# Kernel tuning notes

Measured on AMD Instinct MI355X. Metric: run time of the kernel, lower is better.

## Reference

```python
import jax, jax.numpy as jnp
import numpy as np


def mha(x, mask, wq, bq, wk, bk, wv, bv, wo, bo, n_heads):
    # Flaubert/XLM MultiHeadAttention (eval mode, dropout = identity).
    bs, qlen, dim = x.shape
    dph = dim // n_heads

    def split_heads(t):  # (bs, qlen, dim) -> (bs, n_heads, qlen, dph)
        return t.reshape(bs, qlen, n_heads, dph).transpose(0, 2, 1, 3)

    q = split_heads(x @ wq + bq) / jnp.sqrt(jnp.asarray(dph, x.dtype))
    k = split_heads(x @ wk + bk)
    v = split_heads(x @ wv + bv)

    scores = jnp.einsum('bhqd,bhkd->bhqk', q, k)  # (bs, h, qlen, klen)
    neg = jnp.finfo(scores.dtype).min
    scores = jnp.where((mask == 0)[:, None, None, :], neg, scores)
    weights = jax.nn.softmax(scores, axis=-1)
    ctx = jnp.einsum('bhqk,bhkd->bhqd', weights, v)
    ctx = ctx.transpose(0, 2, 1, 3).reshape(bs, qlen, dim)
    return ctx @ wo + bo


def setup_inputs() -> dict:
    key = jax.random.key(0)
    ks = jax.random.split(key, 20)
    bs, slen = 4, 1024
    d0, d1 = 192, 66
    std = 0.02
    inp = {
        'x': jax.random.normal(ks[0], (bs, slen, d0), jnp.float32),
        'y': jax.random.normal(ks[1], (bs, slen, d1), jnp.float32),
        'mask0': jax.random.randint(ks[2], (bs, slen), 0, 2, jnp.int32),
        'mask1': jax.random.randint(ks[3], (bs, slen), 0, 2, jnp.int32),
    }
    names0 = ['q0', 'k0', 'v0', 'o0']
    names1 = ['q1', 'k1', 'v1', 'o1']
    for i, n in enumerate(names0):
        inp[n + '_w'] = jax.random.normal(ks[4 + i], (d0, d0), jnp.float32) * std
        inp[n + '_b'] = jnp.zeros((d0,), jnp.float32)
    for i, n in enumerate(names1):
        inp[n + '_w'] = jax.random.normal(ks[8 + i], (d1, d1), jnp.float32) * std
        inp[n + '_b'] = jnp.zeros((d1,), jnp.float32)
    return inp


def reference(x, y, mask0, mask1,
              q0_w, q0_b, k0_w, k0_b, v0_w, v0_b, o0_w, o0_b,
              q1_w, q1_b, k1_w, k1_b, v1_w, v1_b, o1_w, o1_b):
    out0 = mha(x, mask0, q0_w, q0_b, k0_w, k0_b, v0_w, v0_b, o0_w, o0_b, n_heads=16)
    out1 = mha(y, mask1, q1_w, q1_b, k1_w, k1_b, v1_w, v1_b, o1_w, o1_b, n_heads=11)
    return (out0, out1)
```

## Files before the change

kernel.cpp:

```cpp
#include <hip/hip_runtime.h>
#include <math.h>


#define BS 4
#define SLEN 1024

#define Q0_OFF 0
#define C0_OFF 786432
#define Q1_OFF 1572864
#define C1_OFF 1843200
#define K0H_OFF 2113536
#define V0T_OFF 2506752
#define K1H_OFF 2899968
#define V1T_OFF 3080192
#define CMAP0_OFF 3215360
#define CMAP1_OFF 3219456
#define CNT_OFF 3223552

#define OUT0_SIZE 786432

#if __has_builtin(__builtin_amdgcn_exp2f)
#define EXP2(x) __builtin_amdgcn_exp2f(x)
#else
#define EXP2(x) __expf((x) * 0.69314718056f)
#endif

typedef _Float16 f16x2 __attribute__((ext_vector_type(2)));
typedef _Float16 f16x4 __attribute__((ext_vector_type(4)));
typedef _Float16 f16x8 __attribute__((ext_vector_type(8)));
typedef float f32x4 __attribute__((ext_vector_type(4)));

union F16x8U { f16x8 v8; f16x4 v4[2]; };

__global__ __launch_bounds__(256) void compact_kernel(
    const int* __restrict__ mask0, const int* __restrict__ mask1,
    int* __restrict__ cmap0, int* __restrict__ cmap1, int* __restrict__ cnts)
{
  __shared__ int sS[256];
  __shared__ int sTot;
  const int inst = blockIdx.x >> 2, b = blockIdx.x & 3;
  const int* m = (inst ? mask1 : mask0) + b * SLEN;
  int* cmap = (inst ? cmap1 : cmap0) + b * SLEN;
  const int tid = threadIdx.x;

  int mv[4], s4 = 0;
#pragma unroll
  for (int i = 0; i < 4; ++i) { mv[i] = m[tid * 4 + i] ? 1 : 0; s4 += mv[i]; }
  sS[tid] = s4;
  __syncthreads();
  for (int off = 1; off < 256; off <<= 1) {
    const int v = sS[tid];
    const int add = (tid >= off) ? sS[tid - off] : 0;
    __syncthreads();
    sS[tid] = v + add;
    __syncthreads();
  }
  if (tid == 255) sTot = sS[255];
  __syncthreads();
  const int tot = sTot;
  int u = tid ? sS[tid - 1] : 0;
#pragma unroll
  for (int i = 0; i < 4; ++i) {
    const int s = tid * 4 + i;
    cmap[s] = mv[i] ? u : tot + (s - u);
    u += mv[i];
  }
  if (tid == 0) cnts[blockIdx.x] = tot;
}

__device__ __forceinline__ void mfma_chunk(const _Float16* sA, const _Float16* sWT,
                                           int wv, int lane, f32x4 acc[4])
{
  const int col = lane & 15, grp = lane >> 4;
#pragma unroll
  for (int ks = 0; ks < 2; ++ks) {
    const f16x8 bf = *(const f16x8*)(sWT + (wv * 16 + col) * 72 + ks * 32 + grp * 8);
#pragma unroll
    for (int mt = 0; mt < 4; ++mt) {
      const f16x8 af = *(const f16x8*)(sA + (mt * 16 + col) * 72 + ks * 32 + grp * 8);
      acc[mt] = __builtin_amdgcn_mfma_f32_16x16x32_f16(af, bf, acc[mt], 0, 0, 0);
    }
  }
}

__device__ __forceinline__ void mfma_chunk_split(
    const _Float16* sAh, const _Float16* sAl,
    const _Float16* sWTh, const _Float16* sWTl,
    int wv, int lane, f32x4 acc[4])
{
  const int col = lane & 15, grp = lane >> 4;
#pragma unroll
  for (int ks = 0; ks < 2; ++ks) {
    const int boff = (wv * 16 + col) * 72 + ks * 32 + grp * 8;
    const f16x8 bh = *(const f16x8*)(sWTh + boff);
    const f16x8 bl = *(const f16x8*)(sWTl + boff);
#pragma unroll
    for (int mt = 0; mt < 4; ++mt) {
      const int aoff = (mt * 16 + col) * 72 + ks * 32 + grp * 8;
      const f16x8 ah = *(const f16x8*)(sAh + aoff);
      const f16x8 al = *(const f16x8*)(sAl + aoff);
      acc[mt] = __builtin_amdgcn_mfma_f32_16x16x32_f16(ah, bh, acc[mt], 0, 0, 0);
      acc[mt] = __builtin_amdgcn_mfma_f32_16x16x32_f16(ah, bl, acc[mt], 0, 0, 0);
      acc[mt] = __builtin_amdgcn_mfma_f32_16x16x32_f16(al, bh, acc[mt], 0, 0, 0);
    }
  }
}

template <int DIM>
__device__ __forceinline__ void stage_chunk(const float* __restrict__ A, int row0,
                                            int kc, const float* __restrict__ W,
                                            int col0, _Float16* sA, _Float16* sWT,
                                            int tid)
{
  for (int idx = tid; idx < 2048; idx += 256) {
    const int m = idx >> 5, k = (idx & 31) * 2;
    float2 v = make_float2(0.f, 0.f);
    if (kc + k < DIM) v = *(const float2*)(A + (size_t)(row0 + m) * DIM + kc + k);
    *(f16x2*)(sA + m * 72 + k) = (f16x2){(_Float16)v.x, (_Float16)v.y};
  }
  for (int idx = tid; idx < 2048; idx += 256) {
    const int k = idx >> 5, n = (idx & 31) * 2;
    float2 v = make_float2(0.f, 0.f);
    if (kc + k < DIM && col0 + n < DIM)
      v = *(const float2*)(W + (size_t)(kc + k) * DIM + col0 + n);
    sWT[n * 72 + k] = (_Float16)v.x;
    sWT[(n + 1) * 72 + k] = (_Float16)v.y;
  }
}

template <int DIM>
__device__ __forceinline__ void stage_chunk_split(
    const float* __restrict__ A, int row0, int kc,
    const float* __restrict__ W, int col0,
    _Float16* sAh, _Float16* sAl, _Float16* sWTh, _Float16* sWTl, int tid)
{
  for (int idx = tid; idx < 2048; idx += 256) {
    const int m = idx >> 5, k = (idx & 31) * 2;
    float2 v = make_float2(0.f, 0.f);
    if (kc + k < DIM) v = *(const float2*)(A + (size_t)(row0 + m) * DIM + kc + k);
    const _Float16 hx = (_Float16)v.x, hy = (_Float16)v.y;
    *(f16x2*)(sAh + m * 72 + k) = (f16x2){hx, hy};
    *(f16x2*)(sAl + m * 72 + k) =
        (f16x2){(_Float16)(v.x - (float)hx), (_Float16)(v.y - (float)hy)};
  }
  for (int idx = tid; idx < 2048; idx += 256) {
    const int k = idx >> 5, n = (idx & 31) * 2;
    float2 v = make_float2(0.f, 0.f);
    if (kc + k < DIM && col0 + n < DIM)
      v = *(const float2*)(W + (size_t)(kc + k) * DIM + col0 + n);
    const _Float16 hx = (_Float16)v.x, hy = (_Float16)v.y;
    sWTh[n * 72 + k] = hx;
    sWTh[(n + 1) * 72 + k] = hy;
    sWTl[n * 72 + k] = (_Float16)(v.x - (float)hx);
    sWTl[(n + 1) * 72 + k] = (_Float16)(v.y - (float)hy);
  }
}

template <int DIM, int H, int DPH, int NT, int NCH, int KST>
__device__ void qkv_impl(int bid, const float* __restrict__ X,
                         const float* __restrict__ qw, const float* __restrict__ qb,
                         const float* __restrict__ kw, const float* __restrict__ kb,
                         const float* __restrict__ vw, const float* __restrict__ vb,
                         float* __restrict__ qo, _Float16* __restrict__ kh,
                         _Float16* __restrict__ vth, const int* __restrict__ cmap,
                         char* smem)
{
  const int mt64 = bid & 63;
  const int rest = bid >> 6;
  const int mat = rest / NT;
  const int nt = rest % NT;
  const int row0 = mt64 * 64, col0 = nt * 64;

  const float* W = (mat == 0) ? qw : (mat == 1) ? kw : vw;
  const float* B = (mat == 0) ? qb : (mat == 1) ? kb : vb;
  const float scale = (mat == 0) ? (1.44269504089f / sqrtf((float)DPH)) : 1.0f;

  _Float16* sA = (_Float16*)smem;
  _Float16* sWT = sA + 64 * 72;

  const int tid = threadIdx.x;
  const int wv = tid >> 6, lane = tid & 63;
  f32x4 acc[4] = {{0.f,0.f,0.f,0.f},{0.f,0.f,0.f,0.f},{0.f,0.f,0.f,0.f},{0.f,0.f,0.f,0.f}};

  for (int c = 0; c < NCH; ++c) {
    __syncthreads();
    stage_chunk<DIM>(X, row0, c * 64, W, col0, sA, sWT, tid);
    __syncthreads();
    mfma_chunk(sA, sWT, wv, lane, acc);
  }

  const int col = lane & 15, grp = lane >> 4;
  const int cidx = col0 + wv * 16 + col;
  if (cidx < DIM) {
    const float bias = B[cidx];
    const int h = cidx / DPH, d = cidx % DPH;
#pragma unroll
    for (int mt = 0; mt < 4; ++mt) {
#pragma unroll
      for (int r = 0; r < 4; ++r) {
        const int m = row0 + mt * 16 + grp * 4 + r;
        const int b = m >> 10, s = m & 1023;
        const float v = acc[mt][r] + bias;
        const int bh = b * H + h;
        if (mat == 0) {
          qo[(size_t)((bh << 10) + s) * DPH + d] = v * scale;
        } else {
          const int sp = cmap[(b << 10) + s];
          if (mat == 1)
            kh[(size_t)((bh << 10) + sp) * KST + d] = (_Float16)v;
          else
            vth[((size_t)(bh * DPH + d) << 10) + sp] = (_Float16)v;
        }
      }
    }
  }
}

__global__ __launch_bounds__(256) void qkv_kernel(
    const float* __restrict__ x, const float* __restrict__ y,
    const float* __restrict__ q0w, const float* __restrict__ q0b,
    const float* __restrict__ k0w, const float* __restrict__ k0b,
    const float* __restrict__ v0w, const float* __restrict__ v0b,
    const float* __restrict__ q1w, const float* __restrict__ q1b,
    const float* __restrict__ k1w, const float* __restrict__ k1b,
    const float* __restrict__ v1w, const float* __restrict__ v1b,
    float* __restrict__ ws)
{
  extern __shared__ char smem[];
  _Float16* hws = (_Float16*)ws;
  const int* cmap0 = (const int*)(ws + CMAP0_OFF);
  const int* cmap1 = (const int*)(ws + CMAP1_OFF);
  const int bid = blockIdx.x;
  if (bid < 576)
    qkv_impl<192, 16, 12, 3, 3, 12>(bid, x, q0w, q0b, k0w, k0b, v0w, v0b,
                                    ws + Q0_OFF, hws + 2 * (size_t)K0H_OFF,
                                    hws + 2 * (size_t)V0T_OFF, cmap0, smem);
  else
    qkv_impl<66, 11, 6, 2, 2, 8>(bid - 576, y, q1w, q1b, k1w, k1b, v1w, v1b,
                                 ws + Q1_OFF, hws + 2 * (size_t)K1H_OFF,
                                 hws + 2 * (size_t)V1T_OFF, cmap1, smem);
}

template <int H, int DPH, int SKP>
__device__ void attn_impl(int bid, const float* __restrict__ qg,
                          const _Float16* __restrict__ kh,
                          const _Float16* __restrict__ vth,
                          const int* __restrict__ cnts,
                          float* __restrict__ ctx, char* smem)
{
  constexpr int CH = 128;
  constexpr int KBUF = CH * SKP + 32;
  constexpr int VST = 136;

  _Float16* sK = (_Float16*)smem;
  _Float16* sVT = sK + 2 * KBUF;

  const int bh = bid >> 4;
  const int b = bh / H;
  const int h = bh % H;
  const int tid = threadIdx.x;

  const float* qb_ = qg + (size_t)bh * SLEN * DPH;
  const _Float16* kb_ = kh + (size_t)bh * SLEN * SKP;
  const _Float16* vb_ = vth + ((size_t)bh * DPH << 10);
  const int cnt = cnts[b];
  const int nch = (cnt + CH - 1) >> 7;

  if (tid < 64) sK[(tid >> 5) * KBUF + CH * SKP + (tid & 31)] = (_Float16)0.f;

  const int wave = tid >> 6, lane = tid & 63;
  const int col = lane & 15, grp = lane >> 4;
  const int qtile = (bid & 15) * 4 + wave;

  f16x4 aq;
  {
    const int qrow = qtile * 16 + col;
#pragma unroll
    for (int j = 0; j < 4; ++j) {
      const int d = grp * 4 + j;
      aq[j] = (d < DPH) ? (_Float16)qb_[(size_t)qrow * DPH + d] : (_Float16)0.f;
    }
  }

  constexpr int kN = CH * SKP / 8;
  constexpr int vN = DPH * 16;
  const int vd = tid >> 4, vq = tid & 15;
  uint4 pk, pv;
  auto prefetch = [&](int cc) {
    if (tid < kN) pk = ((const uint4*)(kb_ + (size_t)cc * CH * SKP))[tid];
    if (tid < vN) pv = ((const uint4*)(vb_ + ((size_t)vd << 10) + cc * CH))[vq];
  };
  auto commit = [&](int pb) {
    if (tid < kN) ((uint4*)(sK + pb * KBUF))[tid] = pk;
    if (tid < vN) *(uint4*)(sVT + (pb * DPH + vd) * VST + vq * 8) = pv;
  };

  prefetch(0);
  commit(0);
  __syncthreads();

  f32x4 Oacc[2] = {{0.f,0.f,0.f,0.f},{0.f,0.f,0.f,0.f}};
  float lsum = 0.f;
  const int de = (col < DPH) ? col : 0;

#pragma unroll 1
  for (int c = 0; c < nch; ++c) {
    const int p = c & 1;
    if (c + 1 < nch) prefetch(c + 1);

    const _Float16* sKp = sK + p * KBUF;
    const _Float16* sVp = sVT + p * DPH * VST;
    const int keyr = c * CH + grp * 4;

#pragma unroll
    for (int kt = 0; kt < CH / 16; ++kt) {
      const f16x4 kf = *(const f16x4*)(sKp + (kt * 16 + col) * SKP + grp * 4);
      const int k0 = keyr + kt * 16;
      const f32x4 biasv = {(k0 < cnt) ? 0.f : -100.f,
                           (k0 + 1 < cnt) ? 0.f : -100.f,
                           (k0 + 2 < cnt) ? 0.f : -100.f,
                           (k0 + 3 < cnt) ? 0.f : -100.f};
      const f32x4 S = __builtin_amdgcn_mfma_f32_16x16x16f16(kf, aq, biasv,
                                                            0, 0, 0);
      const float e0 = EXP2(S[0]), e1 = EXP2(S[1]);
      const float e2 = EXP2(S[2]), e3 = EXP2(S[3]);
      lsum += (e0 + e1) + (e2 + e3);
      const f16x4 pf = {(_Float16)e0, (_Float16)e1, (_Float16)e2, (_Float16)e3};
      const f16x4 vf = *(const f16x4*)(sVp + de * VST + kt * 16 + grp * 4);
      Oacc[kt & 1] = __builtin_amdgcn_mfma_f32_16x16x16f16(pf, vf, Oacc[kt & 1],
                                                           0, 0, 0);
    }

    if (c + 1 < nch) commit(p ^ 1);
    __syncthreads();
  }

  f32x4 Osum;
#pragma unroll
  for (int r = 0; r < 4; ++r) Osum[r] = Oacc[0][r] + Oacc[1][r];
  float lred = lsum;
  lred += __shfl_xor(lred, 16);
  lred += __shfl_xor(lred, 32);
  float lq[4];
#pragma unroll
  for (int r = 0; r < 4; ++r) lq[r] = __shfl(lred, grp * 4 + r);
  if (col < DPH) {
    const int qrow0 = qtile * 16;
#pragma unroll
    for (int r = 0; r < 4; ++r) {
      const int row = qrow0 + grp * 4 + r;
      ctx[(size_t)(b * SLEN + row) * (H * DPH) + h * DPH + col] = Osum[r] / lq[r];
    }
  }
}

__global__ __launch_bounds__(256) void attn_kernel(float* __restrict__ ws)
{
  extern __shared__ char smem[];
  _Float16* hws = (_Float16*)ws;
  const int* cnts = (const int*)(ws + CNT_OFF);
  const int bid = blockIdx.x;
  if (bid < 1024)
    attn_impl<16, 12, 12>(bid, ws + Q0_OFF, hws + 2 * (size_t)K0H_OFF,
                          hws + 2 * (size_t)V0T_OFF, cnts, ws + C0_OFF, smem);
  else
    attn_impl<11, 6, 8>(bid - 1024, ws + Q1_OFF, hws + 2 * (size_t)K1H_OFF,
                        hws + 2 * (size_t)V1T_OFF, cnts + 4, ws + C1_OFF, smem);
}

template <int DIM, int NCH>
__device__ void oproj_impl(int bid, const float* __restrict__ Cx,
                           const float* __restrict__ ow, const float* __restrict__ ob,
                           float* __restrict__ out, char* smem)
{
  const int mt64 = bid & 63;
  const int nt = bid >> 6;
  const int row0 = mt64 * 64, col0 = nt * 64;

  _Float16* sAh = (_Float16*)smem;
  _Float16* sAl = sAh + 64 * 72;
  _Float16* sWTh = sAl + 64 * 72;
  _Float16* sWTl = sWTh + 64 * 72;

  const int tid = threadIdx.x;
  const int wv = tid >> 6, lane = tid & 63;
  f32x4 acc[4] = {{0.f,0.f,0.f,0.f},{0.f,0.f,0.f,0.f},{0.f,0.f,0.f,0.f},{0.f,0.f,0.f,0.f}};

  for (int c = 0; c < NCH; ++c) {
    __syncthreads();
    stage_chunk_split<DIM>(Cx, row0, c * 64, ow, col0, sAh, sAl, sWTh, sWTl, tid);
    __syncthreads();
    mfma_chunk_split(sAh, sAl, sWTh, sWTl, wv, lane, acc);
  }

  const int col = lane & 15, grp = lane >> 4;
  const int cidx = col0 + wv * 16 + col;
  if (cidx < DIM) {
    const float bias = ob[cidx];
#pragma unroll
    for (int mt = 0; mt < 4; ++mt) {
#pragma unroll
      for (int r = 0; r < 4; ++r) {
        const int m = row0 + mt * 16 + grp * 4 + r;
        out[(size_t)m * DIM + cidx] = acc[mt][r] + bias;
      }
    }
  }
}

__global__ __launch_bounds__(256) void oproj_kernel(
    const float* __restrict__ o0w, const float* __restrict__ o0b,
    const float* __restrict__ o1w, const float* __restrict__ o1b,
    float* __restrict__ ws, float* __restrict__ out)
{
  extern __shared__ char smem[];
  const int bid = blockIdx.x;
  if (bid < 192)
    oproj_impl<192, 3>(bid, ws + C0_OFF, o0w, o0b, out, smem);
  else
    oproj_impl<66, 2>(bid - 192, ws + C1_OFF, o1w, o1b, out + OUT0_SIZE, smem);
}

extern "C" void kernel_launch(void* const* d_in, const int* in_sizes, int n_in,
                              void* d_out, int out_size, void* d_ws, size_t ws_size,
                              hipStream_t stream)
{
  const float* x = (const float*)d_in[0];
  const float* y = (const float*)d_in[1];
  const int* mask0 = (const int*)d_in[2];
  const int* mask1 = (const int*)d_in[3];
  const float* q0w = (const float*)d_in[4];  const float* q0b = (const float*)d_in[5];
  const float* k0w = (const float*)d_in[6];  const float* k0b = (const float*)d_in[7];
  const float* v0w = (const float*)d_in[8];  const float* v0b = (const float*)d_in[9];
  const float* o0w = (const float*)d_in[10]; const float* o0b = (const float*)d_in[11];
  const float* q1w = (const float*)d_in[12]; const float* q1b = (const float*)d_in[13];
  const float* k1w = (const float*)d_in[14]; const float* k1b = (const float*)d_in[15];
  const float* v1w = (const float*)d_in[16]; const float* v1b = (const float*)d_in[17];
  const float* o1w = (const float*)d_in[18]; const float* o1b = (const float*)d_in[19];

  float* ws = (float*)d_ws;
  float* out = (float*)d_out;

  const int qkv_smem = 2 * 64 * 72 * 2;
  const int oproj_smem = 4 * 64 * 72 * 2;
  const int attn_smem = 2 * (128 * 12 + 32) * 2 + 2 * 12 * 136 * 2;

  compact_kernel<<<8, 256, 0, stream>>>(mask0, mask1,
                                        (int*)(ws + CMAP0_OFF),
                                        (int*)(ws + CMAP1_OFF),
                                        (int*)(ws + CNT_OFF));
  qkv_kernel<<<960, 256, qkv_smem, stream>>>(x, y, q0w, q0b, k0w, k0b, v0w, v0b,
                                             q1w, q1b, k1w, k1b, v1w, v1b, ws);
  attn_kernel<<<1728, 256, attn_smem, stream>>>(ws);
  oproj_kernel<<<320, 256, oproj_smem, stream>>>(o0w, o0b, o1w, o1b, ws, out);
}
```

Baseline: 156.1 us.

## Fuse all four phases into one persistent cooperative kernel with grid syncs

```diff
diff --git a/kernel.cpp b/kernel.cpp
--- a/kernel.cpp
+++ b/kernel.cpp
@@ -1,5 +1,8 @@
 #include <hip/hip_runtime.h>
+#include <hip/hip_cooperative_groups.h>
 #include <math.h>
+
+namespace cg = cooperative_groups;
 
 
 #define BS 4
@@ -19,6 +22,8 @@
 
 #define OUT0_SIZE 786432
 
+#define FUSED_SMEM 36864
+
 #if __has_builtin(__builtin_amdgcn_exp2f)
 #define EXP2(x) __builtin_amdgcn_exp2f(x)
 #else
@@ -32,13 +37,12 @@
 
 union F16x8U { f16x8 v8; f16x4 v4[2]; };
 
-__global__ __launch_bounds__(256) void compact_kernel(
-    const int* __restrict__ mask0, const int* __restrict__ mask1,
-    int* __restrict__ cmap0, int* __restrict__ cmap1, int* __restrict__ cnts)
-{
-  __shared__ int sS[256];
-  __shared__ int sTot;
-  const int inst = blockIdx.x >> 2, b = blockIdx.x & 3;
+__device__ void compact_phase(int item, const int* __restrict__ mask0,
+                              const int* __restrict__ mask1,
+                              int* __restrict__ cmap0, int* __restrict__ cmap1,
+                              int* __restrict__ cnts, int* sS, int* sTot)
+{
+  const int inst = item >> 2, b = item & 3;
   const int* m = (inst ? mask1 : mask0) + b * SLEN;
   int* cmap = (inst ? cmap1 : cmap0) + b * SLEN;
   const int tid = threadIdx.x;
@@ -55,9 +59,9 @@
     sS[tid] = v + add;
     __syncthreads();
   }
-  if (tid == 255) sTot = sS[255];
+  if (tid == 255) *sTot = sS[255];
   __syncthreads();
-  const int tot = sTot;
+  const int tot = *sTot;
   int u = tid ? sS[tid - 1] : 0;
 #pragma unroll
   for (int i = 0; i < 4; ++i) {
@@ -65,7 +69,17 @@
     cmap[s] = mv[i] ? u : tot + (s - u);
     u += mv[i];
   }
-  if (tid == 0) cnts[blockIdx.x] = tot;
+  if (tid == 0) cnts[item] = tot;
+  __syncthreads();
+}
+
+__global__ __launch_bounds__(256) void compact_kernel(
+    const int* __restrict__ mask0, const int* __restrict__ mask1,
+    int* __restrict__ cmap0, int* __restrict__ cmap1, int* __restrict__ cnts)
+{
+  __shared__ int sS[256];
+  __shared__ int sTot;
+  compact_phase(blockIdx.x, mask0, mask1, cmap0, cmap1, cnts, sS, &sTot);
 }
 
 __device__ __forceinline__ void mfma_chunk(const _Float16* sA, const _Float16* sWT,
@@ -421,6 +435,66 @@
     oproj_impl<66, 2>(bid - 192, ws + C1_OFF, o1w, o1b, out + OUT0_SIZE, smem);
 }
 
+struct FusedParams {
+  const float *x, *y;
+  const int *mask0, *mask1;
+  const float *q0w, *q0b, *k0w, *k0b, *v0w, *v0b, *o0w, *o0b;
+  const float *q1w, *q1b, *k1w, *k1b, *v1w, *v1b, *o1w, *o1b;
+  float* ws;
+  float* out;
+};
+
+__global__ __launch_bounds__(256, 4) void fused_kernel(FusedParams p)
+{
+  extern __shared__ char smem[];
+  float* ws = p.ws;
+  _Float16* hws = (_Float16*)ws;
+  const int bid = blockIdx.x;
+  const int G = gridDim.x;
+  cg::grid_group grid = cg::this_grid();
+
+  int* cmap0 = (int*)(ws + CMAP0_OFF);
+  int* cmap1 = (int*)(ws + CMAP1_OFF);
+  int* cnts = (int*)(ws + CNT_OFF);
+
+  for (int it = bid; it < 8; it += G)
+    compact_phase(it, p.mask0, p.mask1, cmap0, cmap1, cnts,
+                  (int*)smem, (int*)smem + 256);
+  grid.sync();
+
+  for (int it = bid; it < 960; it += G) {
+    if (it < 576)
+      qkv_impl<192, 16, 12, 3, 3, 12>(it, p.x, p.q0w, p.q0b, p.k0w, p.k0b,
+                                      p.v0w, p.v0b, ws + Q0_OFF,
+                                      hws + 2 * (size_t)K0H_OFF,
+                                      hws + 2 * (size_t)V0T_OFF, cmap0, smem);
+    else
+      qkv_impl<66, 11, 6, 2, 2, 8>(it - 576, p.y, p.q1w, p.q1b, p.k1w, p.k1b,
+                                   p.v1w, p.v1b, ws + Q1_OFF,
+                                   hws + 2 * (size_t)K1H_OFF,
+                                   hws + 2 * (size_t)V1T_OFF, cmap1, smem);
+  }
+  grid.sync();
+
+  for (int it = bid; it < 1728; it += G) {
+    if (it < 1024)
+      attn_impl<16, 12, 12>(it, ws + Q0_OFF, hws + 2 * (size_t)K0H_OFF,
+                            hws + 2 * (size_t)V0T_OFF, cnts, ws + C0_OFF, smem);
+    else
+      attn_impl<11, 6, 8>(it - 1024, ws + Q1_OFF, hws + 2 * (size_t)K1H_OFF,
+                          hws + 2 * (size_t)V1T_OFF, cnts + 4, ws + C1_OFF, smem);
+  }
+  grid.sync();
+
+  for (int it = bid; it < 320; it += G) {
+    if (it < 192)
+      oproj_impl<192, 3>(it, ws + C0_OFF, p.o0w, p.o0b, p.out, smem);
+    else
+      oproj_impl<66, 2>(it - 192, ws + C1_OFF, p.o1w, p.o1b, p.out + OUT0_SIZE,
+                        smem);
+  }
+}
+
 extern "C" void kernel_launch(void* const* d_in, const int* in_sizes, int n_in,
                               void* d_out, int out_size, void* d_ws, size_t ws_size,
                               hipStream_t stream)
@@ -441,6 +515,23 @@
   float* ws = (float*)d_ws;
   float* out = (float*)d_out;
 
+  FusedParams p = {x, y, mask0, mask1,
+                   q0w, q0b, k0w, k0b, v0w, v0b, o0w, o0b,
+                   q1w, q1b, k1w, k1b, v1w, v1b, o1w, o1b,
+                   ws, out};
+  int nb = 0;
+  hipError_t occ = hipOccupancyMaxActiveBlocksPerMultiprocessor(
+      &nb, fused_kernel, 256, (size_t)FUSED_SMEM);
+  if (occ == hipSuccess && nb >= 1) {
+    int grid = nb * 256;
+    if (grid > 1728) grid = 1728;
+    void* args[] = {(void*)&p};
+    hipError_t e = hipLaunchCooperativeKernel(fused_kernel, dim3(grid),
+                                              dim3(256), args,
+                                              (unsigned)FUSED_SMEM, stream);
+    if (e == hipSuccess) return;
+  }
+
   const int qkv_smem = 2 * 64 * 72 * 2;
   const int oproj_smem = 4 * 64 * 72 * 2;
   const int attn_smem = 2 * (128 * 12 + 32) * 2 + 2 * 12 * 136 * 2;
```

New measurement: 315.2 us. +101.9%, slower.

## Fuse mask compaction into QKV kernel and register-prefetch GEMM staging chunks

Applied to the files above, without the earlier changes.

```diff
diff --git a/kernel.cpp b/kernel.cpp
--- a/kernel.cpp
+++ b/kernel.cpp
@@ -13,8 +13,6 @@
 #define V0T_OFF 2506752
 #define K1H_OFF 2899968
 #define V1T_OFF 3080192
-#define CMAP0_OFF 3215360
-#define CMAP1_OFF 3219456
 #define CNT_OFF 3223552
 
 #define OUT0_SIZE 786432
@@ -29,44 +27,6 @@
 typedef _Float16 f16x4 __attribute__((ext_vector_type(4)));
 typedef _Float16 f16x8 __attribute__((ext_vector_type(8)));
 typedef float f32x4 __attribute__((ext_vector_type(4)));
-
-union F16x8U { f16x8 v8; f16x4 v4[2]; };
-
-__global__ __launch_bounds__(256) void compact_kernel(
-    const int* __restrict__ mask0, const int* __restrict__ mask1,
-    int* __restrict__ cmap0, int* __restrict__ cmap1, int* __restrict__ cnts)
-{
-  __shared__ int sS[256];
-  __shared__ int sTot;
-  const int inst = blockIdx.x >> 2, b = blockIdx.x & 3;
-  const int* m = (inst ? mask1 : mask0) + b * SLEN;
-  int* cmap = (inst ? cmap1 : cmap0) + b * SLEN;
-  const int tid = threadIdx.x;
-
-  int mv[4], s4 = 0;
-#pragma unroll
-  for (int i = 0; i < 4; ++i) { mv[i] = m[tid * 4 + i] ? 1 : 0; s4 += mv[i]; }
-  sS[tid] = s4;
-  __syncthreads();
-  for (int off = 1; off < 256; off <<= 1) {
-    const int v = sS[tid];
-    const int add = (tid >= off) ? sS[tid - off] : 0;
-    __syncthreads();
-    sS[tid] = v + add;
-    __syncthreads();
-  }
-  if (tid == 255) sTot = sS[255];
-  __syncthreads();
-  const int tot = sTot;
-  int u = tid ? sS[tid - 1] : 0;
-#pragma unroll
-  for (int i = 0; i < 4; ++i) {
-    const int s = tid * 4 + i;
-    cmap[s] = mv[i] ? u : tot + (s - u);
-    u += mv[i];
-  }
-  if (tid == 0) cnts[blockIdx.x] = tot;
-}
 
 __device__ __forceinline__ void mfma_chunk(const _Float16* sA, const _Float16* sWT,
                                            int wv, int lane, f32x4 acc[4])
@@ -106,63 +66,14 @@
   }
 }
 
-template <int DIM>
-__device__ __forceinline__ void stage_chunk(const float* __restrict__ A, int row0,
-                                            int kc, const float* __restrict__ W,
-                                            int col0, _Float16* sA, _Float16* sWT,
-                                            int tid)
-{
-  for (int idx = tid; idx < 2048; idx += 256) {
-    const int m = idx >> 5, k = (idx & 31) * 2;
-    float2 v = make_float2(0.f, 0.f);
-    if (kc + k < DIM) v = *(const float2*)(A + (size_t)(row0 + m) * DIM + kc + k);
-    *(f16x2*)(sA + m * 72 + k) = (f16x2){(_Float16)v.x, (_Float16)v.y};
-  }
-  for (int idx = tid; idx < 2048; idx += 256) {
-    const int k = idx >> 5, n = (idx & 31) * 2;
-    float2 v = make_float2(0.f, 0.f);
-    if (kc + k < DIM && col0 + n < DIM)
-      v = *(const float2*)(W + (size_t)(kc + k) * DIM + col0 + n);
-    sWT[n * 72 + k] = (_Float16)v.x;
-    sWT[(n + 1) * 72 + k] = (_Float16)v.y;
-  }
-}
-
-template <int DIM>
-__device__ __forceinline__ void stage_chunk_split(
-    const float* __restrict__ A, int row0, int kc,
-    const float* __restrict__ W, int col0,
-    _Float16* sAh, _Float16* sAl, _Float16* sWTh, _Float16* sWTl, int tid)
-{
-  for (int idx = tid; idx < 2048; idx += 256) {
-    const int m = idx >> 5, k = (idx & 31) * 2;
-    float2 v = make_float2(0.f, 0.f);
-    if (kc + k < DIM) v = *(const float2*)(A + (size_t)(row0 + m) * DIM + kc + k);
-    const _Float16 hx = (_Float16)v.x, hy = (_Float16)v.y;
-    *(f16x2*)(sAh + m * 72 + k) = (f16x2){hx, hy};
-    *(f16x2*)(sAl + m * 72 + k) =
-        (f16x2){(_Float16)(v.x - (float)hx), (_Float16)(v.y - (float)hy)};
-  }
-  for (int idx = tid; idx < 2048; idx += 256) {
-    const int k = idx >> 5, n = (idx & 31) * 2;
-    float2 v = make_float2(0.f, 0.f);
-    if (kc + k < DIM && col0 + n < DIM)
-      v = *(const float2*)(W + (size_t)(kc + k) * DIM + col0 + n);
-    const _Float16 hx = (_Float16)v.x, hy = (_Float16)v.y;
-    sWTh[n * 72 + k] = hx;
-    sWTh[(n + 1) * 72 + k] = hy;
-    sWTl[n * 72 + k] = (_Float16)(v.x - (float)hx);
-    sWTl[(n + 1) * 72 + k] = (_Float16)(v.y - (float)hy);
-  }
-}
-
 template <int DIM, int H, int DPH, int NT, int NCH, int KST>
 __device__ void qkv_impl(int bid, const float* __restrict__ X,
+                         const int* __restrict__ mask,
                          const float* __restrict__ qw, const float* __restrict__ qb,
                          const float* __restrict__ kw, const float* __restrict__ kb,
                          const float* __restrict__ vw, const float* __restrict__ vb,
                          float* __restrict__ qo, _Float16* __restrict__ kh,
-                         _Float16* __restrict__ vth, const int* __restrict__ cmap,
+                         _Float16* __restrict__ vth, int* __restrict__ cnt_out,
                          char* smem)
 {
   const int mt64 = bid & 63;
@@ -177,15 +88,87 @@
 
   _Float16* sA = (_Float16*)smem;
   _Float16* sWT = sA + 64 * 72;
+  int* sSP = (int*)(smem + 2 * 64 * 72 * 2);
 
   const int tid = threadIdx.x;
   const int wv = tid >> 6, lane = tid & 63;
+
+  float2 rA[8], rW[8];
+  auto qprefetch = [&](int c) {
+    const int kc = c * 64;
+#pragma unroll
+    for (int t = 0; t < 8; ++t) {
+      const int idx = tid + t * 256;
+      {
+        const int m = idx >> 5, k = (idx & 31) * 2;
+        rA[t] = (kc + k < DIM)
+                    ? *(const float2*)(X + (size_t)(row0 + m) * DIM + kc + k)
+                    : make_float2(0.f, 0.f);
+      }
+      {
+        const int k = idx >> 5, n = (idx & 31) * 2;
+        rW[t] = (kc + k < DIM && col0 + n < DIM)
+                    ? *(const float2*)(W + (size_t)(kc + k) * DIM + col0 + n)
+                    : make_float2(0.f, 0.f);
+      }
+    }
+  };
+  auto qcommit = [&]() {
+#pragma unroll
+    for (int t = 0; t < 8; ++t) {
+      const int idx = tid + t * 256;
+      {
+        const int m = idx >> 5, k = (idx & 31) * 2;
+        *(f16x2*)(sA + m * 72 + k) = (f16x2){(_Float16)rA[t].x, (_Float16)rA[t].y};
+      }
+      {
+        const int k = idx >> 5, n = (idx & 31) * 2;
+        sWT[n * 72 + k] = (_Float16)rW[t].x;
+        sWT[(n + 1) * 72 + k] = (_Float16)rW[t].y;
+      }
+    }
+  };
+
+  qprefetch(0);
+
+  if (mat != 0) {
+    int* sS = (int*)smem;
+    const int b = row0 >> 10;
+    const int* m = mask + (b << 10);
+    int mv[4], s4 = 0;
+#pragma unroll
+    for (int i = 0; i < 4; ++i) { mv[i] = m[tid * 4 + i] ? 1 : 0; s4 += mv[i]; }
+    sS[tid] = s4;
+    __syncthreads();
+    for (int off = 1; off < 256; off <<= 1) {
+      const int v = sS[tid];
+      const int add = (tid >= off) ? sS[tid - off] : 0;
+      __syncthreads();
+      sS[tid] = v + add;
+      __syncthreads();
+    }
+    const int tot = sS[255];
+    int u = tid ? sS[tid - 1] : 0;
+    const int s0 = row0 & 1023;
+#pragma unroll
+    for (int i = 0; i < 4; ++i) {
+      const int s = tid * 4 + i;
+      const int sp = mv[i] ? u : tot + (s - u);
+      u += mv[i];
+      const unsigned rel = (unsigned)(s - s0);
+      if (rel < 64u) sSP[rel] = sp;
+    }
+    if (mat == 1 && nt == 0 && s0 == 0 && tid == 0) cnt_out[b] = tot;
+    __syncthreads();
+  }
+
   f32x4 acc[4] = {{0.f,0.f,0.f,0.f},{0.f,0.f,0.f,0.f},{0.f,0.f,0.f,0.f},{0.f,0.f,0.f,0.f}};
 
   for (int c = 0; c < NCH; ++c) {
     __syncthreads();
-    stage_chunk<DIM>(X, row0, c * 64, W, col0, sA, sWT, tid);
-    __syncthreads();
+    qcommit();
+    __syncthreads();
+    if (c + 1 < NCH) qprefetch(c + 1);
     mfma_chunk(sA, sWT, wv, lane, acc);
   }
 
@@ -205,7 +188,7 @@
         if (mat == 0) {
           qo[(size_t)((bh << 10) + s) * DPH + d] = v * scale;
         } else {
-          const int sp = cmap[(b << 10) + s];
+          const int sp = sSP[mt * 16 + grp * 4 + r];
           if (mat == 1)
             kh[(size_t)((bh << 10) + sp) * KST + d] = (_Float16)v;
           else
@@ -218,6 +201,7 @@
 
 __global__ __launch_bounds__(256) void qkv_kernel(
     const float* __restrict__ x, const float* __restrict__ y,
+    const int* __restrict__ mask0, const int* __restrict__ mask1,
     const float* __restrict__ q0w, const float* __restrict__ q0b,
     const float* __restrict__ k0w, const float* __restrict__ k0b,
     const float* __restrict__ v0w, const float* __restrict__ v0b,
@@ -228,17 +212,16 @@
 {
   extern __shared__ char smem[];
   _Float16* hws = (_Float16*)ws;
-  const int* cmap0 = (const int*)(ws + CMAP0_OFF);
-  const int* cmap1 = (const int*)(ws + CMAP1_OFF);
+  int* cnts = (int*)(ws + CNT_OFF);
   const int bid = blockIdx.x;
   if (bid < 576)
-    qkv_impl<192, 16, 12, 3, 3, 12>(bid, x, q0w, q0b, k0w, k0b, v0w, v0b,
+    qkv_impl<192, 16, 12, 3, 3, 12>(bid, x, mask0, q0w, q0b, k0w, k0b, v0w, v0b,
                                     ws + Q0_OFF, hws + 2 * (size_t)K0H_OFF,
-                                    hws + 2 * (size_t)V0T_OFF, cmap0, smem);
+                                    hws + 2 * (size_t)V0T_OFF, cnts, smem);
   else
-    qkv_impl<66, 11, 6, 2, 2, 8>(bid - 576, y, q1w, q1b, k1w, k1b, v1w, v1b,
+    qkv_impl<66, 11, 6, 2, 2, 8>(bid - 576, y, mask1, q1w, q1b, k1w, k1b, v1w, v1b,
                                  ws + Q1_OFF, hws + 2 * (size_t)K1H_OFF,
-                                 hws + 2 * (size_t)V1T_OFF, cmap1, smem);
+                                 hws + 2 * (size_t)V1T_OFF, cnts + 4, smem);
 }
 
 template <int H, int DPH, int SKP>
@@ -384,12 +367,58 @@
 
   const int tid = threadIdx.x;
   const int wv = tid >> 6, lane = tid & 63;
+
+  float2 rA[8], rW[8];
+  auto oprefetch = [&](int c) {
+    const int kc = c * 64;
+#pragma unroll
+    for (int t = 0; t < 8; ++t) {
+      const int idx = tid + t * 256;
+      {
+        const int m = idx >> 5, k = (idx & 31) * 2;
+        rA[t] = (kc + k < DIM)
+                    ? *(const float2*)(Cx + (size_t)(row0 + m) * DIM + kc + k)
+                    : make_float2(0.f, 0.f);
+      }
+      {
+        const int k = idx >> 5, n = (idx & 31) * 2;
+        rW[t] = (kc + k < DIM && col0 + n < DIM)
+                    ? *(const float2*)(ow + (size_t)(kc + k) * DIM + col0 + n)
+                    : make_float2(0.f, 0.f);
+      }
+    }
+  };
+  auto ocommit = [&]() {
+#pragma unroll
+    for (int t = 0; t < 8; ++t) {
+      const int idx = tid + t * 256;
+      {
+        const int m = idx >> 5, k = (idx & 31) * 2;
+        const _Float16 hx = (_Float16)rA[t].x, hy = (_Float16)rA[t].y;
+        *(f16x2*)(sAh + m * 72 + k) = (f16x2){hx, hy};
+        *(f16x2*)(sAl + m * 72 + k) =
+            (f16x2){(_Float16)(rA[t].x - (float)hx), (_Float16)(rA[t].y - (float)hy)};
+      }
+      {
+        const int k = idx >> 5, n = (idx & 31) * 2;
+        const _Float16 hx = (_Float16)rW[t].x, hy = (_Float16)rW[t].y;
+        sWTh[n * 72 + k] = hx;
+        sWTh[(n + 1) * 72 + k] = hy;
+        sWTl[n * 72 + k] = (_Float16)(rW[t].x - (float)hx);
+        sWTl[(n + 1) * 72 + k] = (_Float16)(rW[t].y - (float)hy);
+      }
+    }
+  };
+
+  oprefetch(0);
+
   f32x4 acc[4] = {{0.f,0.f,0.f,0.f},{0.f,0.f,0.f,0.f},{0.f,0.f,0.f,0.f},{0.f,0.f,0.f,0.f}};
 
   for (int c = 0; c < NCH; ++c) {
     __syncthreads();
-    stage_chunk_split<DIM>(Cx, row0, c * 64, ow, col0, sAh, sAl, sWTh, sWTl, tid);
-    __syncthreads();
+    ocommit();
+    __syncthreads();
+    if (c + 1 < NCH) oprefetch(c + 1);
     mfma_chunk_split(sAh, sAl, sWTh, sWTl, wv, lane, acc);
   }
 
@@ -441,15 +470,12 @@
   float* ws = (float*)d_ws;
   float* out = (float*)d_out;
 
-  const int qkv_smem = 2 * 64 * 72 * 2;
+  const int qkv_smem = 2 * 64 * 72 * 2 + 64 * 4;
   const int oproj_smem = 4 * 64 * 72 * 2;
   const int attn_smem = 2 * (128 * 12 + 32) * 2 + 2 * 12 * 136 * 2;
 
-  compact_kernel<<<8, 256, 0, stream>>>(mask0, mask1,
-                                        (int*)(ws + CMAP0_OFF),
-                                        (int*)(ws + CMAP1_OFF),
-                                        (int*)(ws + CNT_OFF));
-  qkv_kernel<<<960, 256, qkv_smem, stream>>>(x, y, q0w, q0b, k0w, k0b, v0w, v0b,
+  qkv_kernel<<<960, 256, qkv_smem, stream>>>(x, y, mask0, mask1,
+                                             q0w, q0b, k0w, k0b, v0w, v0b,
                                              q1w, q1b, k1w, k1b, v1w, v1b, ws);
   attn_kernel<<<1728, 256, attn_smem, stream>>>(ws);
   oproj_kernel<<<320, 256, oproj_smem, stream>>>(o0w, o0b, o1w, o1b, ws, out);
```

Result: faster. 144.4 us (-7.5%).
